# Kernel tuning notes

Measured on AMD Instinct MI355X. Metric: run time of the kernel, lower is better.

## Reference

```python
import jax, jax.numpy as jnp
import numpy as np

NG = 1024      # graphs
NPG = 128      # nodes per graph (forced by lin1 = Linear(128*hid, 128))
N = NG * NPG   # 131072 nodes
DEG = 16       # avg in-graph degree
E = N * DEG    # 2,097,152 edges
IN, H = 4, 64


def setup_inputs() -> dict:
    key = jax.random.key(0)
    ks = jax.random.split(key, 24)
    x = jax.random.normal(ks[0], (N, IN), jnp.float32)
    # edges constrained within each 128-node graph
    src = jax.random.randint(ks[1], (E,), 0, NPG)
    dst = jax.random.randint(ks[2], (E,), 0, NPG)
    off = jnp.repeat(jnp.arange(NG, dtype=jnp.int32) * NPG, NPG * DEG)
    edge_index = jnp.stack([src.astype(jnp.int32) + off, dst.astype(jnp.int32) + off])
    g = lambda k, shp, fan: jax.random.normal(k, shp, jnp.float32) / np.float32(np.sqrt(fan))
    return {
        "x": x, "edge_index": edge_index,
        # GATv2Conv(4->64)
        "Wl": g(ks[3], (IN, H), IN), "bl": jnp.zeros((H,), jnp.float32),
        "Wr": g(ks[4], (IN, H), IN), "br": jnp.zeros((H,), jnp.float32),
        "att_v2": g(ks[5], (H,), H), "b_v2": jnp.zeros((H,), jnp.float32),
        # GATConv #1 (64->64)
        "Wg1": g(ks[6], (H, H), H), "as1": g(ks[7], (H,), H),
        "ad1": g(ks[8], (H,), H), "bg1": jnp.zeros((H,), jnp.float32),
        # GATConv #2 (64->64)
        "Wg2": g(ks[9], (H, H), H), "as2": g(ks[10], (H,), H),
        "ad2": g(ks[11], (H,), H), "bg2": jnp.zeros((H,), jnp.float32),
        # LayerNorm(64)
        "ln_g": jnp.ones((H,), jnp.float32), "ln_b": jnp.zeros((H,), jnp.float32),
        # heads: Linear(128*64 -> 128), Linear(128 -> 1)
        "W1": g(ks[12], (NPG * H, 128), NPG * H), "b1": jnp.zeros((128,), jnp.float32),
        "W2": g(ks[13], (128, 1), 128), "b2": jnp.zeros((1,), jnp.float32),
    }


def _seg_softmax(logits, seg):
    # stable softmax over edges grouped by destination node
    m = jax.ops.segment_max(logits, seg, num_segments=N)
    ex = jnp.exp(logits - m[seg])
    s = jax.ops.segment_sum(ex, seg, num_segments=N)
    return ex / (s[seg] + 1e-16)


def _gatv2(x, src, dst, Wl, bl, Wr, br, att, bias):
    xl = x @ Wl + bl                       # source transform [N,H]
    xr = x @ Wr + br                       # target transform [N,H]
    e = jax.nn.leaky_relu(xl[src] + xr[dst], 0.2) @ att   # [E]
    a = _seg_softmax(e, dst)
    out = jax.ops.segment_sum(a[:, None] * xl[src], dst, num_segments=N)
    return out + bias


def _gat(x, src, dst, W, a_src, a_dst, bias):
    # GATConv default: add self-loops
    loop = jnp.arange(N, dtype=src.dtype)
    s2 = jnp.concatenate([src, loop]); d2 = jnp.concatenate([dst, loop])
    xw = x @ W                             # [N,H]
    al_s = xw @ a_src; al_d = xw @ a_dst   # per-node attention halves [N]
    e = jax.nn.leaky_relu(al_s[s2] + al_d[d2], 0.2)
    a = _seg_softmax(e, d2)
    out = jax.ops.segment_sum(a[:, None] * xw[s2], d2, num_segments=N)
    return out + bias


def _layernorm(x, g, b, eps=1e-5):
    mu = jnp.mean(x, -1, keepdims=True)
    var = jnp.mean(jnp.square(x - mu), -1, keepdims=True)
    return (x - mu) * jax.lax.rsqrt(var + eps) * g + b


def reference(x, edge_index, Wl, bl, Wr, br, att_v2, b_v2,
              Wg1, as1, ad1, bg1, Wg2, as2, ad2, bg2,
              ln_g, ln_b, W1, b1, W2, b2):
    src, dst = edge_index[0], edge_index[1]
    h = jax.nn.leaky_relu(_gatv2(x, src, dst, Wl, bl, Wr, br, att_v2, b_v2), 0.01)
    h = _layernorm(h, ln_g, ln_b)
    h = jax.nn.relu(_gat(h, src, dst, Wg1, as1, ad1, bg1))
    h = jax.nn.relu(_gat(h, src, dst, Wg2, as2, ad2, bg2))
    # linearize: batch is sorted with exactly NPG nodes per graph -> reshape
    h = h.reshape(NG, NPG * H)
    h = jax.nn.leaky_relu(h @ W1 + b1, 0.01)
    return jax.nn.sigmoid(h @ W2 + b2)     # [NG, 1]
```

## Files before the change

### kernel.cpp

```cpp
#include <hip/hip_runtime.h>
#include <hip/hip_bf16.h>

#define NGRAPH 1024
#define NPG 128
#define NTOT (NGRAPH*NPG)
#define EPG 2048
#define ETOT (NTOT*16)
#define HD 64

typedef unsigned int uint;
typedef unsigned short ushort_t;
typedef __attribute__((ext_vector_type(8))) short s8v;
typedef __attribute__((ext_vector_type(4))) float f32x4;

#define MFMA16 __builtin_amdgcn_mfma_f32_16x16x32_bf16

__device__ __forceinline__ float lrelu(float x, float s){ return fmaxf(x, x*s); }
__device__ __forceinline__ float b2lo(uint u){ return __uint_as_float(u << 16); }
__device__ __forceinline__ float b2hi(uint u){ return __uint_as_float(u & 0xFFFF0000u); }
__device__ __forceinline__ uint pkbf(float a, float b){
  union { __hip_bfloat162 h; uint u; } t;
  t.h = __hip_bfloat162{__float2bfloat16(a), __float2bfloat16(b)};
  return t.u;
}
__device__ __forceinline__ ushort_t bfb(float v){
  __hip_bfloat16 h = __float2bfloat16(v);
  union { __hip_bfloat16 h; ushort_t u; } t; t.h = h; return t.u;
}
union U4S8 { uint4 u; s8v s; };
__device__ __forceinline__ s8v bcs8(uint4 u){ U4S8 t; t.u = u; return t.s; }
__device__ __forceinline__ s8v pk8(uint4 x, uint4 y){
  U4S8 t;
  t.u.x = pkbf(__uint_as_float(x.x), __uint_as_float(x.y));
  t.u.y = pkbf(__uint_as_float(x.z), __uint_as_float(x.w));
  t.u.z = pkbf(__uint_as_float(y.x), __uint_as_float(y.y));
  t.u.w = pkbf(__uint_as_float(y.z), __uint_as_float(y.w));
  return t.s;
}

#define DPP_ADD(v, ctrl) ((v) + __int_as_float(__builtin_amdgcn_update_dpp(0, __float_as_int(v), (ctrl), 0xF, 0xF, false)))

__device__ __forceinline__ int oswz(int r, int p){ return (r<<5) | ((((p>>2) ^ (r & 7))<<2) | (p & 3)); }
__device__ __forceinline__ int obase(int r, int oc){ return (r<<5) | (((oc) ^ (r & 7))<<2); }
__device__ __forceinline__ int t64(int r, int p){ return (r<<6) | ((((p>>2) ^ (r & 15))<<2) | (p & 3)); }
__device__ __forceinline__ int t64b(int r, int q){ return (r<<6) | (((q ^ (r & 15))<<2)); }
__device__ __forceinline__ int fP(int r, int k){ return (r<<7) | (((((k>>2) ^ r) & 31)<<2) | (k & 3)); }
__device__ __forceinline__ int fPb(int r, int q){ return (r<<7) | ((((q ^ r) & 31))<<2); }

#define O_A   0
#define O_B   4096
#define O_P   8192
#define O_E   12288
#define O_ED  14336
#define O_SOF 15360
#define O_SPO 15489
#define O_NMV 15617
#define O_SSE 15745
#define O_ALS 15873
#define O_ALD 16001
#define O_WAS 16132
#define O_WAD 16196
#define SM_SZ 16260

__global__ __launch_bounds__(256) void gnn_fused(
    const float* __restrict__ x, const int* __restrict__ ei,
    const float* __restrict__ Wl, const float* __restrict__ bl,
    const float* __restrict__ Wr, const float* __restrict__ br,
    const float* __restrict__ att, const float* __restrict__ bv2,
    const float* __restrict__ Wg1, const float* __restrict__ as1,
    const float* __restrict__ ad1, const float* __restrict__ bg1,
    const float* __restrict__ Wg2, const float* __restrict__ as2,
    const float* __restrict__ ad2, const float* __restrict__ bg2,
    const float* __restrict__ lng, const float* __restrict__ lnb,
    uint* __restrict__ hout)
{
  __shared__ uint SM[SM_SZ];
  uint*     sXl  = SM + O_A;
  uint*     sXr  = SM + O_B;
  float*    Pf   = (float*)(SM + O_P);
  float*    eva  = (float*)(SM + O_E);
  ushort_t* edsd = (ushort_t*)(SM + O_ED);
  int*      soff = (int*)(SM + O_SOF);
  int*      spos = (int*)(SM + O_SPO);
  float*    nmv  = (float*)(SM + O_NMV);
  float*    sse  = (float*)(SM + O_SSE);
  float*    als  = (float*)(SM + O_ALS);
  float*    ald  = (float*)(SM + O_ALD);
  float*    was  = (float*)(SM + O_WAS);
  float*    wad  = (float*)(SM + O_WAD);
  ushort_t* sH16 = (ushort_t*)(SM + O_A);
  ushort_t* sT16 = (ushort_t*)(SM + O_B);
  ushort_t* wg16 = (ushort_t*)(SM + O_E);

  const int g    = blockIdx.x;
  const int tid  = threadIdx.x;
  const int lane = tid & 63;
  const int wv   = tid >> 6;
  const int lw   = lane & 15;
  const int lq   = lane >> 4;
  const int oc   = lane & 7;
  const int ebase = g * EPG;

  if (tid < NPG) spos[tid] = 0;
  __syncthreads();
  for (int e = tid; e < EPG; e += 256)
    atomicAdd(&spos[ei[ETOT + ebase + e] - g*NPG], 1);
  __syncthreads();
  if (wv == 0) {
    int c0 = spos[lane], c1 = spos[lane + 64];
    #pragma unroll
    for (int o = 1; o < 64; o <<= 1) { int t = __shfl_up(c0, o); if (lane >= o) c0 += t; }
    #pragma unroll
    for (int o = 1; o < 64; o <<= 1) { int t = __shfl_up(c1, o); if (lane >= o) c1 += t; }
    int tot0 = __shfl(c0, 63);
    soff[lane + 1]  = c0;
    soff[lane + 65] = c1 + tot0;
    if (lane == 0) soff[0] = 0;
  }
  __syncthreads();
  if (tid < NPG) spos[tid] = soff[tid];
  __syncthreads();
  for (int e = tid; e < EPG; e += 256) {
    int s = ei[ebase + e] - g*NPG;
    int d = ei[ETOT + ebase + e] - g*NPG;
    int p = atomicAdd(&spos[d], 1);
    edsd[p] = (ushort_t)(s | (d << 8));
  }

  {
    const int pl = lane & 31, hb = lane >> 5;
    const float2 wl0 = *(const float2*)&Wl[0*64 + 2*pl];
    const float2 wl1 = *(const float2*)&Wl[1*64 + 2*pl];
    const float2 wl2 = *(const float2*)&Wl[2*64 + 2*pl];
    const float2 wl3 = *(const float2*)&Wl[3*64 + 2*pl];
    const float2 wr0 = *(const float2*)&Wr[0*64 + 2*pl];
    const float2 wr1 = *(const float2*)&Wr[1*64 + 2*pl];
    const float2 wr2 = *(const float2*)&Wr[2*64 + 2*pl];
    const float2 wr3 = *(const float2*)&Wr[3*64 + 2*pl];
    const float2 blp = *(const float2*)&bl[2*pl];
    const float2 brp = *(const float2*)&br[2*pl];
    const float4* x4 = (const float4*)x + (size_t)g * NPG;
    __syncthreads();
    for (int st = 0; st < 16; st++) {
      int i = st*8 + wv*2 + hb;
      float4 xi = x4[i];
      float l0 = blp.x + xi.x*wl0.x + xi.y*wl1.x + xi.z*wl2.x + xi.w*wl3.x;
      float l1 = blp.y + xi.x*wl0.y + xi.y*wl1.y + xi.z*wl2.y + xi.w*wl3.y;
      float r0 = brp.x + xi.x*wr0.x + xi.y*wr1.x + xi.z*wr2.x + xi.w*wr3.x;
      float r1 = brp.y + xi.x*wr0.y + xi.y*wr1.y + xi.z*wr2.y + xi.w*wr3.y;
      sXl[oswz(i, pl)] = pkbf(l0, l1);
      sXr[oswz(i, pl)] = pkbf(r0, r1);
    }
  }
  __syncthreads();

  {
    const int grp = lane >> 3;
    float4 atA = *(const float4*)&att[oc*8];
    float4 atB = *(const float4*)&att[oc*8 + 4];
    int base = wv * 512;
    for (int stp = 0; stp < 64; stp++) {
      int e  = base + stp*8 + grp;
      int sd = edsd[e];
      int s  = sd & 127, d = sd >> 8;
      uint4 ql = *(uint4*)&sXl[obase(s, oc)];
      uint4 qr = *(uint4*)&sXr[obase(d, oc)];
      float acc, v;
      v = b2lo(ql.x)+b2lo(qr.x); acc  = lrelu(v,0.2f)*atA.x;
      v = b2hi(ql.x)+b2hi(qr.x); acc += lrelu(v,0.2f)*atA.y;
      v = b2lo(ql.y)+b2lo(qr.y); acc += lrelu(v,0.2f)*atA.z;
      v = b2hi(ql.y)+b2hi(qr.y); acc += lrelu(v,0.2f)*atA.w;
      v = b2lo(ql.z)+b2lo(qr.z); acc += lrelu(v,0.2f)*atB.x;
      v = b2hi(ql.z)+b2hi(qr.z); acc += lrelu(v,0.2f)*atB.y;
      v = b2lo(ql.w)+b2lo(qr.w); acc += lrelu(v,0.2f)*atB.z;
      v = b2hi(ql.w)+b2hi(qr.w); acc += lrelu(v,0.2f)*atB.w;
      acc = DPP_ADD(acc, 0x111); acc = DPP_ADD(acc, 0x112); acc = DPP_ADD(acc, 0x114);
      if ((lane & 7) == 7) eva[e] = acc;
    }
  }
  __syncthreads();

  {
    const int g16 = tid >> 4, sl = tid & 15;
    for (int it = 0; it < 8; it++) {
      int d = it*16 + g16;
      int p0 = soff[d], p1 = soff[d+1];
      float m = -1e30f;
      for (int p = p0 + sl; p < p1; p += 16) m = fmaxf(m, eva[p]);
      #pragma unroll
      for (int o = 1; o < 16; o <<= 1) m = fmaxf(m, __shfl_xor(m, o));
      float ssum = 0.f;
      for (int p = p0 + sl; p < p1; p += 16) {
        float ex = __expf(eva[p] - m); ssum += ex; eva[p] = ex;
      }
      #pragma unroll
      for (int o = 1; o < 16; o <<= 1) ssum += __shfl_xor(ssum, o);
      if (sl == 0) nmv[d] = 1.f / (ssum + 1e-16f);
    }
    ushort_t* xl16 = (ushort_t*)(SM + O_A);
    int j = tid & 63, spb = tid >> 6;
    for (int i = 0; i < 16; i++) {
      int sp = spb*16 + i;
      float v0 = __uint_as_float((uint)xl16[oswz(2*sp,   j>>1)*2 + (j&1)] << 16);
      float v1 = __uint_as_float((uint)xl16[oswz(2*sp+1, j>>1)*2 + (j&1)] << 16);
      sXr[t64(j, sp)] = pkbf(v0, v1);
    }
  }
  __syncthreads();

  {
    int n0 = 32*(wv>>1), m0 = 16*(wv&1);
    float bja = bv2[n0 + lw], bjb = bv2[n0 + 16 + lw];
    for (int q = 0; q < 4; q++) {
      #pragma unroll
      for (int i = 0; i < 4; i++) { uint4 z = {0,0,0,0}; *(uint4*)&SM[O_P + (tid + i*256)*4] = z; }
      __syncthreads();
      int p0 = soff[q*32], p1 = soff[q*32 + 32];
      for (int p = p0 + tid; p < p1; p += 256) {
        int sd = edsd[p]; int s = sd & 127, d = sd >> 8;
        atomicAdd(&Pf[fP(d - q*32, s)], eva[p] * nmv[d]);
      }
      __syncthreads();
      f32x4 c0 = {0.f,0.f,0.f,0.f}, c1 = {0.f,0.f,0.f,0.f};
      int row = m0 + lw;
      #pragma unroll
      for (int ks = 0; ks < 4; ks++) {
        int kk = ks*32 + lq*8;
        uint4 f0 = *(uint4*)&Pf[fPb(row, kk>>2)];
        uint4 f1 = *(uint4*)&Pf[fPb(row, (kk>>2)+1)];
        s8v a = pk8(f0, f1);
        s8v b0 = bcs8(*(uint4*)&SM[O_B + t64b(n0 + lw,      kk>>3)]);
        s8v b1 = bcs8(*(uint4*)&SM[O_B + t64b(n0 + 16 + lw, kk>>3)]);
        c0 = MFMA16(a, b0, c0, 0, 0, 0);
        c1 = MFMA16(a, b1, c1, 0, 0, 0);
      }
      int rg0 = q*32 + m0 + lq*4;
      #pragma unroll
      for (int rg = 0; rg < 4; rg++) {
        float v0 = lrelu(c0[rg] + bja, 0.01f);
        float v1 = lrelu(c1[rg] + bjb, 0.01f);
        int jc0 = n0 + lw, jc1 = n0 + 16 + lw;
        sH16[oswz(rg0+rg, jc0>>1)*2 + (jc0&1)] = bfb(v0);
        sH16[oswz(rg0+rg, jc1>>1)*2 + (jc1&1)] = bfb(v1);
      }
      __syncthreads();
    }
  }

  {
    int pl = lane & 31, hb = lane >> 5;
    float2 gv = *(const float2*)&lng[2*pl];
    float2 bv = *(const float2*)&lnb[2*pl];
    for (int it = 0; it < 16; it++) {
      int d = it*8 + wv*2 + hb;
      uint w = SM[O_A + oswz(d, pl)];
      float v0 = b2lo(w), v1 = b2hi(w);
      float s1 = v0 + v1, s2 = v0*v0 + v1*v1;
      #pragma unroll
      for (int o = 1; o < 32; o <<= 1) { s1 += __shfl_xor(s1, o); s2 += __shfl_xor(s2, o); }
      float mu  = s1 * 0.015625f;
      float var = s2 * 0.015625f - mu*mu;
      float rs  = rsqrtf(var + 1e-5f);
      v0 = (v0 - mu)*rs*gv.x + bv.x;
      v1 = (v1 - mu)*rs*gv.y + bv.y;
      SM[O_A + oswz(d, pl)] = pkbf(v0, v1);
    }
  }
  __syncthreads();

  for (int layer = 0; layer < 2; layer++) {
    const float* Wg  = layer ? Wg2 : Wg1;
    const float* avs = layer ? as2 : as1;
    const float* avd = layer ? ad2 : ad1;
    const float* bg  = layer ? bg2 : bg1;

    if (tid < 128) {
      const float* av = (tid < 64) ? avs : avd;
      float* dst = (tid < 64) ? was : wad;
      int k = tid & 63;
      float acc = 0.f;
      #pragma unroll
      for (int jj = 0; jj < 16; jj++) {
        float4 w = *(const float4*)&Wg[k*64 + jj*4];
        float4 a = *(const float4*)&av[jj*4];
        acc += w.x*a.x + w.y*a.y + w.z*a.z + w.w*a.w;
      }
      dst[k] = acc;
    } else {
      int t2 = tid - 128;
      #pragma unroll
      for (int i = 0; i < 8; i++) {
        int idx = t2 + i*128;
        int k = idx >> 4, j4 = (idx & 15)*4;
        float4 w = *(const float4*)&Wg[k*64 + j4];
        wg16[oswz(j4+0, k>>1)*2 + (k&1)] = bfb(w.x);
        wg16[oswz(j4+1, k>>1)*2 + (k&1)] = bfb(w.y);
        wg16[oswz(j4+2, k>>1)*2 + (k&1)] = bfb(w.z);
        wg16[oswz(j4+3, k>>1)*2 + (k&1)] = bfb(w.w);
      }
    }
    __syncthreads();

    {
      int row = 16*wv + lw;
      s8v a0 = bcs8(*(uint4*)&SM[O_E + obase(row, lq)]);
      s8v a1 = bcs8(*(uint4*)&SM[O_E + obase(row, 4+lq)]);
      #pragma unroll
      for (int nt = 0; nt < 8; nt++) {
        int d = nt*16 + lw;
        s8v b0 = bcs8(*(uint4*)&SM[O_A + obase(d, lq)]);
        s8v b1 = bcs8(*(uint4*)&SM[O_A + obase(d, 4+lq)]);
        f32x4 c = {0.f,0.f,0.f,0.f};
        c = MFMA16(a0, b0, c, 0, 0, 0);
        c = MFMA16(a1, b1, c, 0, 0, 0);
        int j0 = 16*wv + lq*4;
        #pragma unroll
        for (int rg = 0; rg < 4; rg++)
          sT16[t64(j0+rg, d>>1)*2 + (d&1)] = bfb(c[rg]);
      }
    }
    __syncthreads();

    {
      float4 ws0 = *(float4*)&was[oc*8], ws1 = *(float4*)&was[oc*8 + 4];
      float4 wd0 = *(float4*)&wad[oc*8], wd1 = *(float4*)&wad[oc*8 + 4];
      for (int ps = 0; ps < 4; ps++) {
        int n = ps*32 + (tid >> 3);
        uint4 q = *(uint4*)&SM[O_A + obase(n, oc)];
        float f0=b2lo(q.x), f1=b2hi(q.x), f2=b2lo(q.y), f3=b2hi(q.y);
        float f4=b2lo(q.z), f5=b2hi(q.z), f6=b2lo(q.w), f7=b2hi(q.w);
        float sa = f0*ws0.x+f1*ws0.y+f2*ws0.z+f3*ws0.w+f4*ws1.x+f5*ws1.y+f6*ws1.z+f7*ws1.w;
        float sd = f0*wd0.x+f1*wd0.y+f2*wd0.z+f3*wd0.w+f4*wd1.x+f5*wd1.y+f6*wd1.z+f7*wd1.w;
        sa = DPP_ADD(sa, 0x111); sa = DPP_ADD(sa, 0x112); sa = DPP_ADD(sa, 0x114);
        sd = DPP_ADD(sd, 0x111); sd = DPP_ADD(sd, 0x112); sd = DPP_ADD(sd, 0x114);
        if ((lane & 7) == 7) { als[n] = sa; ald[n] = sd; }
      }
    }
    __syncthreads();

    #pragma unroll
    for (int i = 0; i < 8; i++) {
      int e = tid + i*256;
      int sd = edsd[e];
      eva[e] = lrelu(als[sd & 127] + ald[sd >> 8], 0.2f);
    }
    __syncthreads();

    {
      const int g16 = tid >> 4, sl = tid & 15;
      for (int it = 0; it < 8; it++) {
        int d = it*16 + g16;
        int p0 = soff[d], p1 = soff[d+1];
        float se = lrelu(als[d] + ald[d], 0.2f);
        float m = se;
        for (int p = p0 + sl; p < p1; p += 16) m = fmaxf(m, eva[p]);
        #pragma unroll
        for (int o = 1; o < 16; o <<= 1) m = fmaxf(m, __shfl_xor(m, o));
        float ex0 = __expf(se - m);
        float ssum = 0.f;
        for (int p = p0 + sl; p < p1; p += 16) {
          float ex = __expf(eva[p] - m); ssum += ex; eva[p] = ex;
        }
        #pragma unroll
        for (int o = 1; o < 16; o <<= 1) ssum += __shfl_xor(ssum, o);
        if (sl == 0) { nmv[d] = 1.f / (ssum + ex0 + 1e-16f); sse[d] = ex0; }
      }
    }
    __syncthreads();

    {
      int n0 = 32*(wv>>1), m0 = 16*(wv&1);
      float bja = bg[n0 + lw], bjb = bg[n0 + 16 + lw];
      for (int q = 0; q < 4; q++) {
        #pragma unroll
        for (int i = 0; i < 4; i++) { uint4 z = {0,0,0,0}; *(uint4*)&SM[O_P + (tid + i*256)*4] = z; }
        __syncthreads();
        int p0 = soff[q*32], p1 = soff[q*32 + 32];
        for (int p = p0 + tid; p < p1; p += 256) {
          int sd = edsd[p]; int s = sd & 127, d = sd >> 8;
          atomicAdd(&Pf[fP(d - q*32, s)], eva[p] * nmv[d]);
        }
        if (tid < 32) { int d = q*32 + tid; atomicAdd(&Pf[fP(tid, d)], sse[d] * nmv[d]); }
        __syncthreads();
        f32x4 c0 = {0.f,0.f,0.f,0.f}, c1 = {0.f,0.f,0.f,0.f};
        int row = m0 + lw;
        #pragma unroll
        for (int ks = 0; ks < 4; ks++) {
          int kk = ks*32 + lq*8;
          uint4 f0 = *(uint4*)&Pf[fPb(row, kk>>2)];
          uint4 f1 = *(uint4*)&Pf[fPb(row, (kk>>2)+1)];
          s8v a = pk8(f0, f1);
          s8v b0 = bcs8(*(uint4*)&SM[O_B + t64b(n0 + lw,      kk>>3)]);
          s8v b1 = bcs8(*(uint4*)&SM[O_B + t64b(n0 + 16 + lw, kk>>3)]);
          c0 = MFMA16(a, b0, c0, 0, 0, 0);
          c1 = MFMA16(a, b1, c1, 0, 0, 0);
        }
        int rg0 = q*32 + m0 + lq*4;
        #pragma unroll
        for (int rg = 0; rg < 4; rg++) {
          float v0 = fmaxf(c0[rg] + bja, 0.f);
          float v1 = fmaxf(c1[rg] + bjb, 0.f);
          int jc0 = n0 + lw, jc1 = n0 + 16 + lw;
          sH16[oswz(rg0+rg, jc0>>1)*2 + (jc0&1)] = bfb(v0);
          sH16[oswz(rg0+rg, jc1>>1)*2 + (jc1&1)] = bfb(v1);
        }
        __syncthreads();
      }
    }
  }

  {
    uint* hg = hout + (size_t)g * 4096;
    #pragma unroll
    for (int i = 0; i < 16; i++) {
      int idx = tid + i*256;
      hg[idx] = SM[O_A + oswz(idx >> 5, idx & 31)];
    }
  }
}

__global__ __launch_bounds__(256) void w1_transpose(const float* __restrict__ W1,
                                                    uint* __restrict__ w1t)
{
  __shared__ float sw[64*130];
  const int tid = threadIdx.x;
  const int k0 = blockIdx.x * 64;
  #pragma unroll
  for (int i = 0; i < 8; i++) {
    int idx = tid + i*256;
    int r = idx >> 5, c4 = (idx & 31)*4;
    *(float4*)&sw[r*130 + c4] = *(const float4*)&W1[(size_t)(k0+r)*128 + c4];
  }
  __syncthreads();
  #pragma unroll
  for (int i = 0; i < 16; i++) {
    int idx = tid + i*256;
    int c = idx >> 5, kp = idx & 31;
    w1t[(size_t)c*4096 + (k0>>1) + kp] = pkbf(sw[(2*kp)*130 + c], sw[(2*kp+1)*130 + c]);
  }
}

__global__ __launch_bounds__(256) void head_gemm(
    const uint* __restrict__ hbuf, const uint* __restrict__ w1t,
    float* __restrict__ partial)
{
  __shared__ uint sAh[2048];
  __shared__ uint sBh[4096];
  const int tid = threadIdx.x, lane = tid & 63, wv = tid >> 6;
  const int lw = lane & 15, lq = lane >> 4;
  const int g0 = blockIdx.x * 64;
  const int ks = blockIdx.y;
  f32x4 acc[8];
  #pragma unroll
  for (int i = 0; i < 8; i++) acc[i] = f32x4{0.f,0.f,0.f,0.f};

  for (int ch = 0; ch < 8; ch++) {
    int pb = ks*256 + ch*32;
    #pragma unroll
    for (int i = 0; i < 2; i++) {
      int idx = tid + i*256; int r = idx >> 3, q4 = idx & 7;
      uint4 v = *(const uint4*)&hbuf[(size_t)(g0+r)*4096 + pb + q4*4];
      *(uint4*)&sAh[(r<<5) | ((q4 ^ (r & 7))<<2)] = v;
    }
    #pragma unroll
    for (int i = 0; i < 4; i++) {
      int idx = tid + i*256; int r = idx >> 3, q4 = idx & 7;
      uint4 v = *(const uint4*)&w1t[(size_t)r*4096 + pb + q4*4];
      *(uint4*)&sBh[(r<<5) | ((q4 ^ (r & 7))<<2)] = v;
    }
    __syncthreads();
    int ra = 16*wv + lw;
    s8v a0 = bcs8(*(uint4*)&sAh[obase(ra, lq)]);
    s8v a1 = bcs8(*(uint4*)&sAh[obase(ra, 4+lq)]);
    #pragma unroll
    for (int nt = 0; nt < 8; nt++) {
      int c = nt*16 + lw;
      s8v b0 = bcs8(*(uint4*)&sBh[obase(c, lq)]);
      s8v b1 = bcs8(*(uint4*)&sBh[obase(c, 4+lq)]);
      acc[nt] = MFMA16(a0, b0, acc[nt], 0, 0, 0);
      acc[nt] = MFMA16(a1, b1, acc[nt], 0, 0, 0);
    }
    __syncthreads();
  }
  float* pp = partial + (size_t)ks*131072;
  #pragma unroll
  for (int nt = 0; nt < 8; nt++) {
    int c = nt*16 + lw;
    int r0 = g0 + 16*wv + lq*4;
    #pragma unroll
    for (int rg = 0; rg < 4; rg++)
      pp[(size_t)(r0+rg)*128 + c] = acc[nt][rg];
  }
}

__global__ __launch_bounds__(64) void head_out(
    const float* __restrict__ partial, const float* __restrict__ b1,
    const float* __restrict__ W2, const float* __restrict__ b2,
    float* __restrict__ out)
{
  const int g = blockIdx.x;
  const int l = threadIdx.x;
  float v0 = b1[l], v1 = b1[64 + l];
  #pragma unroll
  for (int s = 0; s < 16; s++) {
    v0 += partial[(size_t)s*131072 + g*128 + l];
    v1 += partial[(size_t)s*131072 + g*128 + 64 + l];
  }
  float sum = lrelu(v0, 0.01f)*W2[l] + lrelu(v1, 0.01f)*W2[64 + l];
  #pragma unroll
  for (int m = 32; m > 0; m >>= 1) sum += __shfl_xor(sum, m);
  if (l == 0) out[g] = 1.f / (1.f + __expf(-(sum + b2[0])));
}

extern "C" void kernel_launch(void* const* d_in, const int* in_sizes, int n_in,
                              void* d_out, int out_size, void* d_ws, size_t ws_size,
                              hipStream_t stream) {
  const float* x   = (const float*)d_in[0];
  const int*   ei  = (const int*)  d_in[1];
  const float* Wl  = (const float*)d_in[2];
  const float* bl_ = (const float*)d_in[3];
  const float* Wr  = (const float*)d_in[4];
  const float* br_ = (const float*)d_in[5];
  const float* att = (const float*)d_in[6];
  const float* bv2 = (const float*)d_in[7];
  const float* Wg1 = (const float*)d_in[8];
  const float* as1 = (const float*)d_in[9];
  const float* ad1 = (const float*)d_in[10];
  const float* bg1 = (const float*)d_in[11];
  const float* Wg2 = (const float*)d_in[12];
  const float* as2 = (const float*)d_in[13];
  const float* ad2 = (const float*)d_in[14];
  const float* bg2 = (const float*)d_in[15];
  const float* lng = (const float*)d_in[16];
  const float* lnb = (const float*)d_in[17];
  const float* W1  = (const float*)d_in[18];
  const float* b1  = (const float*)d_in[19];
  const float* W2  = (const float*)d_in[20];
  const float* b2  = (const float*)d_in[21];
  float* out = (float*)d_out;

  uint*  hbuf    = (uint*)d_ws;
  float* partial = (float*)((char*)d_ws + (size_t)16*1024*1024);
  uint*  w1t     = (uint*)((char*)d_ws + (size_t)24*1024*1024);

  w1_transpose<<<128, 256, 0, stream>>>(W1, w1t);
  gnn_fused<<<NGRAPH, 256, 0, stream>>>(x, ei, Wl, bl_, Wr, br_, att, bv2,
      Wg1, as1, ad1, bg1, Wg2, as2, ad2, bg2, lng, lnb, hbuf);
  head_gemm<<<dim3(16, 16), 256, 0, stream>>>(hbuf, w1t, partial);
  head_out<<<NGRAPH, 64, 0, stream>>>(partial, b1, W2, b2, out);
}
```

Baseline: 289.7 us.

## Shrink LDS footprint by spilling sorted edges to global and halving P tile

```diff
diff --git a/kernel.cpp b/kernel.cpp
--- a/kernel.cpp
+++ b/kernel.cpp
@@ -3,9 +3,8 @@
 
 #define NGRAPH 1024
 #define NPG 128
-#define NTOT (NGRAPH*NPG)
 #define EPG 2048
-#define ETOT (NTOT*16)
+#define ETOT (NGRAPH*NPG*16)
 #define HD 64
 
 typedef unsigned int uint;
@@ -24,8 +23,7 @@
   return t.u;
 }
 __device__ __forceinline__ ushort_t bfb(float v){
-  __hip_bfloat16 h = __float2bfloat16(v);
-  union { __hip_bfloat16 h; ushort_t u; } t; t.h = h; return t.u;
+  union { __hip_bfloat16 h; ushort_t u; } t; t.h = __float2bfloat16(v); return t.u;
 }
 union U4S8 { uint4 u; s8v s; };
 __device__ __forceinline__ s8v bcs8(uint4 u){ U4S8 t; t.u = u; return t.s; }
@@ -37,32 +35,68 @@
   t.u.w = pkbf(__uint_as_float(y.z), __uint_as_float(y.w));
   return t.s;
 }
-
 #define DPP_ADD(v, ctrl) ((v) + __int_as_float(__builtin_amdgcn_update_dpp(0, __float_as_int(v), (ctrl), 0xF, 0xF, false)))
 
 __device__ __forceinline__ int oswz(int r, int p){ return (r<<5) | ((((p>>2) ^ (r & 7))<<2) | (p & 3)); }
 __device__ __forceinline__ int obase(int r, int oc){ return (r<<5) | (((oc) ^ (r & 7))<<2); }
 __device__ __forceinline__ int t64(int r, int p){ return (r<<6) | ((((p>>2) ^ (r & 15))<<2) | (p & 3)); }
 __device__ __forceinline__ int t64b(int r, int q){ return (r<<6) | (((q ^ (r & 15))<<2)); }
-__device__ __forceinline__ int fP(int r, int k){ return (r<<7) | (((((k>>2) ^ r) & 31)<<2) | (k & 3)); }
-__device__ __forceinline__ int fPb(int r, int q){ return (r<<7) | ((((q ^ r) & 31))<<2); }
-
-#define O_A   0
-#define O_B   4096
+__device__ __forceinline__ int fP16(int r, int k){ return (r<<7) | (((((k>>2) ^ r) & 31)<<2) | (k & 3)); }
+__device__ __forceinline__ int fP16b(int r, int q){ return (r<<7) | ((((q ^ r) & 31))<<2); }
+
+#define O_H   0
+#define O_T   4096
 #define O_P   8192
-#define O_E   12288
-#define O_ED  14336
-#define O_SOF 15360
-#define O_SPO 15489
-#define O_NMV 15617
-#define O_SSE 15745
-#define O_ALS 15873
-#define O_ALD 16001
-#define O_WAS 16132
-#define O_WAD 16196
-#define SM_SZ 16260
-
-__global__ __launch_bounds__(256) void gnn_fused(
+#define O_E   10240
+#define O_SOF 12288
+#define O_ALS 12353
+#define O_ALD 12481
+#define SM_SZ 12609
+
+__device__ __forceinline__ void aggregate_rounds(
+    uint* SM, const ushort_t* soff16, const float* eva, const ushort_t* edsG,
+    const float* selfw, const float* biasp, bool dorelu,
+    int tid, int wv, int lw, int lq)
+{
+  float* Pf = (float*)(SM + O_P);
+  ushort_t* sH16 = (ushort_t*)(SM + O_H);
+  float bj = biasp[16*wv + lw];
+  for (int q = 0; q < 8; q++) {
+    uint4 z = {0,0,0,0};
+    *(uint4*)&SM[O_P + tid*8]     = z;
+    *(uint4*)&SM[O_P + tid*8 + 4] = z;
+    __syncthreads();
+    int p0 = soff16[q*16], p1 = soff16[q*16 + 16];
+    for (int p = p0 + tid; p < p1; p += 256) {
+      int sd = edsG[p];
+      atomicAdd(&Pf[fP16((sd >> 8) - q*16, sd & 127)], eva[p]);
+    }
+    if (selfw && tid < 16)
+      atomicAdd(&Pf[fP16(tid, q*16 + tid)], selfw[q*16 + tid]);
+    __syncthreads();
+    f32x4 c = {0.f,0.f,0.f,0.f};
+    #pragma unroll
+    for (int ks = 0; ks < 4; ks++) {
+      int kk = ks*32 + lq*8;
+      uint4 f0 = *(uint4*)&Pf[fP16b(lw, (kk>>2))];
+      uint4 f1 = *(uint4*)&Pf[fP16b(lw, (kk>>2)+1)];
+      s8v a = pk8(f0, f1);
+      s8v b = bcs8(*(uint4*)&SM[O_T + t64b(16*wv + lw, kk>>3)]);
+      c = MFMA16(a, b, c, 0, 0, 0);
+    }
+    int col = 16*wv + lw;
+    #pragma unroll
+    for (int rg = 0; rg < 4; rg++) {
+      float v = c[rg] + bj;
+      v = dorelu ? fmaxf(v, 0.f) : lrelu(v, 0.01f);
+      int r = q*16 + lq*4 + rg;
+      sH16[oswz(r, col>>1)*2 + (col&1)] = bfb(v);
+    }
+    __syncthreads();
+  }
+}
+
+__global__ __launch_bounds__(256, 3) void gnn_fused(
     const float* __restrict__ x, const int* __restrict__ ei,
     const float* __restrict__ Wl, const float* __restrict__ bl,
     const float* __restrict__ Wr, const float* __restrict__ br,
@@ -72,25 +106,15 @@
     const float* __restrict__ Wg2, const float* __restrict__ as2,
     const float* __restrict__ ad2, const float* __restrict__ bg2,
     const float* __restrict__ lng, const float* __restrict__ lnb,
-    uint* __restrict__ hout)
+    uint* __restrict__ hout, uint* __restrict__ edsd_ws)
 {
   __shared__ uint SM[SM_SZ];
-  uint*     sXl  = SM + O_A;
-  uint*     sXr  = SM + O_B;
-  float*    Pf   = (float*)(SM + O_P);
-  float*    eva  = (float*)(SM + O_E);
-  ushort_t* edsd = (ushort_t*)(SM + O_ED);
-  int*      soff = (int*)(SM + O_SOF);
-  int*      spos = (int*)(SM + O_SPO);
-  float*    nmv  = (float*)(SM + O_NMV);
-  float*    sse  = (float*)(SM + O_SSE);
-  float*    als  = (float*)(SM + O_ALS);
-  float*    ald  = (float*)(SM + O_ALD);
-  float*    was  = (float*)(SM + O_WAS);
-  float*    wad  = (float*)(SM + O_WAD);
-  ushort_t* sH16 = (ushort_t*)(SM + O_A);
-  ushort_t* sT16 = (ushort_t*)(SM + O_B);
-  ushort_t* wg16 = (ushort_t*)(SM + O_E);
+  float*    eva   = (float*)(SM + O_E);
+  ushort_t* soff16= (ushort_t*)(SM + O_SOF);
+  float*    als   = (float*)(SM + O_ALS);
+  float*    ald   = (float*)(SM + O_ALD);
+  ushort_t* sH16  = (ushort_t*)(SM + O_H);
+  ushort_t* sT16  = (ushort_t*)(SM + O_T);
 
   const int g    = blockIdx.x;
   const int tid  = threadIdx.x;
@@ -100,34 +124,44 @@
   const int lq   = lane >> 4;
   const int oc   = lane & 7;
   const int ebase = g * EPG;
-
-  if (tid < NPG) spos[tid] = 0;
-  __syncthreads();
-  for (int e = tid; e < EPG; e += 256)
-    atomicAdd(&spos[ei[ETOT + ebase + e] - g*NPG], 1);
-  __syncthreads();
-  if (wv == 0) {
-    int c0 = spos[lane], c1 = spos[lane + 64];
-    #pragma unroll
-    for (int o = 1; o < 64; o <<= 1) { int t = __shfl_up(c0, o); if (lane >= o) c0 += t; }
-    #pragma unroll
-    for (int o = 1; o < 64; o <<= 1) { int t = __shfl_up(c1, o); if (lane >= o) c1 += t; }
-    int tot0 = __shfl(c0, 63);
-    soff[lane + 1]  = c0;
-    soff[lane + 65] = c1 + tot0;
-    if (lane == 0) soff[0] = 0;
-  }
-  __syncthreads();
-  if (tid < NPG) spos[tid] = soff[tid];
-  __syncthreads();
-  for (int e = tid; e < EPG; e += 256) {
-    int s = ei[ebase + e] - g*NPG;
-    int d = ei[ETOT + ebase + e] - g*NPG;
-    int p = atomicAdd(&spos[d], 1);
-    edsd[p] = (ushort_t)(s | (d << 8));
-  }
+  uint* eg = edsd_ws + (size_t)g * 1024;
+  const ushort_t* edsG = (const ushort_t*)eg;
 
   {
+    int* spos = (int*)(SM + O_P + 1024);
+    ushort_t* edsL = (ushort_t*)(SM + O_P);
+    if (tid < NPG) spos[tid] = 0;
+    __syncthreads();
+    for (int e = tid; e < EPG; e += 256)
+      atomicAdd(&spos[ei[ETOT + ebase + e] - g*NPG], 1);
+    __syncthreads();
+    if (wv == 0) {
+      int c0 = spos[lane], c1 = spos[lane + 64];
+      #pragma unroll
+      for (int o = 1; o < 64; o <<= 1) { int t = __shfl_up(c0, o); if (lane >= o) c0 += t; }
+      #pragma unroll
+      for (int o = 1; o < 64; o <<= 1) { int t = __shfl_up(c1, o); if (lane >= o) c1 += t; }
+      int tot0 = __shfl(c0, 63);
+      soff16[lane + 1]  = (ushort_t)c0;
+      soff16[lane + 65] = (ushort_t)(c1 + tot0);
+      if (lane == 0) soff16[0] = 0;
+    }
+    __syncthreads();
+    if (tid < NPG) spos[tid] = soff16[tid];
+    __syncthreads();
+    for (int e = tid; e < EPG; e += 256) {
+      int s = ei[ebase + e] - g*NPG;
+      int d = ei[ETOT + ebase + e] - g*NPG;
+      int p = atomicAdd(&spos[d], 1);
+      edsL[p] = (ushort_t)(s | (d << 8));
+    }
+    __syncthreads();
+  }
+
+  {
+    #pragma unroll
+    for (int i = 0; i < 4; i++) eg[tid + i*256] = SM[O_P + tid + i*256];
+
     const int pl = lane & 31, hb = lane >> 5;
     const float2 wl0 = *(const float2*)&Wl[0*64 + 2*pl];
     const float2 wl1 = *(const float2*)&Wl[1*64 + 2*pl];
@@ -140,7 +174,6 @@
     const float2 blp = *(const float2*)&bl[2*pl];
     const float2 brp = *(const float2*)&br[2*pl];
     const float4* x4 = (const float4*)x + (size_t)g * NPG;
-    __syncthreads();
     for (int st = 0; st < 16; st++) {
       int i = st*8 + wv*2 + hb;
       float4 xi = x4[i];
@@ -148,23 +181,24 @@
       float l1 = blp.y + xi.x*wl0.y + xi.y*wl1.y + xi.z*wl2.y + xi.w*wl3.y;
       float r0 = brp.x + xi.x*wr0.x + xi.y*wr1.x + xi.z*wr2.x + xi.w*wr3.x;
       float r1 = brp.y + xi.x*wr0.y + xi.y*wr1.y + xi.z*wr2.y + xi.w*wr3.y;
-      sXl[oswz(i, pl)] = pkbf(l0, l1);
-      sXr[oswz(i, pl)] = pkbf(r0, r1);
+      SM[O_H + oswz(i, pl)] = pkbf(l0, l1);
+      SM[O_T + oswz(i, pl)] = pkbf(r0, r1);
     }
   }
   __syncthreads();
 
   {
     const int grp = lane >> 3;
+    const ushort_t* edsL = (const ushort_t*)(SM + O_P);
     float4 atA = *(const float4*)&att[oc*8];
     float4 atB = *(const float4*)&att[oc*8 + 4];
     int base = wv * 512;
     for (int stp = 0; stp < 64; stp++) {
       int e  = base + stp*8 + grp;
-      int sd = edsd[e];
+      int sd = edsL[e];
       int s  = sd & 127, d = sd >> 8;
-      uint4 ql = *(uint4*)&sXl[obase(s, oc)];
-      uint4 qr = *(uint4*)&sXr[obase(d, oc)];
+      uint4 ql = *(uint4*)&SM[O_H + obase(s, oc)];
+      uint4 qr = *(uint4*)&SM[O_T + obase(d, oc)];
       float acc, v;
       v = b2lo(ql.x)+b2lo(qr.x); acc  = lrelu(v,0.2f)*atA.x;
       v = b2hi(ql.x)+b2hi(qr.x); acc += lrelu(v,0.2f)*atA.y;
@@ -184,68 +218,30 @@
     const int g16 = tid >> 4, sl = tid & 15;
     for (int it = 0; it < 8; it++) {
       int d = it*16 + g16;
-      int p0 = soff[d], p1 = soff[d+1];
+      int p0 = soff16[d], p1 = soff16[d+1];
       float m = -1e30f;
       for (int p = p0 + sl; p < p1; p += 16) m = fmaxf(m, eva[p]);
       #pragma unroll
       for (int o = 1; o < 16; o <<= 1) m = fmaxf(m, __shfl_xor(m, o));
       float ssum = 0.f;
-      for (int p = p0 + sl; p < p1; p += 16) {
-        float ex = __expf(eva[p] - m); ssum += ex; eva[p] = ex;
-      }
+      for (int p = p0 + sl; p < p1; p += 16) { float ex = __expf(eva[p]-m); ssum += ex; eva[p] = ex; }
       #pragma unroll
       for (int o = 1; o < 16; o <<= 1) ssum += __shfl_xor(ssum, o);
-      if (sl == 0) nmv[d] = 1.f / (ssum + 1e-16f);
-    }
-    ushort_t* xl16 = (ushort_t*)(SM + O_A);
+      float rnm = 1.f / (ssum + 1e-16f);
+      for (int p = p0 + sl; p < p1; p += 16) eva[p] *= rnm;
+    }
+    ushort_t* xl16 = (ushort_t*)(SM + O_H);
     int j = tid & 63, spb = tid >> 6;
     for (int i = 0; i < 16; i++) {
       int sp = spb*16 + i;
       float v0 = __uint_as_float((uint)xl16[oswz(2*sp,   j>>1)*2 + (j&1)] << 16);
       float v1 = __uint_as_float((uint)xl16[oswz(2*sp+1, j>>1)*2 + (j&1)] << 16);
-      sXr[t64(j, sp)] = pkbf(v0, v1);
+      SM[O_T + t64(j, sp)] = pkbf(v0, v1);
     }
   }
   __syncthreads();
 
-  {
-    int n0 = 32*(wv>>1), m0 = 16*(wv&1);
-    float bja = bv2[n0 + lw], bjb = bv2[n0 + 16 + lw];
-    for (int q = 0; q < 4; q++) {
-      #pragma unroll
-      for (int i = 0; i < 4; i++) { uint4 z = {0,0,0,0}; *(uint4*)&SM[O_P + (tid + i*256)*4] = z; }
-      __syncthreads();
-      int p0 = soff[q*32], p1 = soff[q*32 + 32];
-      for (int p = p0 + tid; p < p1; p += 256) {
-        int sd = edsd[p]; int s = sd & 127, d = sd >> 8;
-        atomicAdd(&Pf[fP(d - q*32, s)], eva[p] * nmv[d]);
-      }
-      __syncthreads();
-      f32x4 c0 = {0.f,0.f,0.f,0.f}, c1 = {0.f,0.f,0.f,0.f};
-      int row = m0 + lw;
-      #pragma unroll
-      for (int ks = 0; ks < 4; ks++) {
-        int kk = ks*32 + lq*8;
-        uint4 f0 = *(uint4*)&Pf[fPb(row, kk>>2)];
-        uint4 f1 = *(uint4*)&Pf[fPb(row, (kk>>2)+1)];
-        s8v a = pk8(f0, f1);
-        s8v b0 = bcs8(*(uint4*)&SM[O_B + t64b(n0 + lw,      kk>>3)]);
-        s8v b1 = bcs8(*(uint4*)&SM[O_B + t64b(n0 + 16 + lw, kk>>3)]);
-        c0 = MFMA16(a, b0, c0, 0, 0, 0);
-        c1 = MFMA16(a, b1, c1, 0, 0, 0);
-      }
-      int rg0 = q*32 + m0 + lq*4;
-      #pragma unroll
-      for (int rg = 0; rg < 4; rg++) {
-        float v0 = lrelu(c0[rg] + bja, 0.01f);
-        float v1 = lrelu(c1[rg] + bjb, 0.01f);
-        int jc0 = n0 + lw, jc1 = n0 + 16 + lw;
-        sH16[oswz(rg0+rg, jc0>>1)*2 + (jc0&1)] = bfb(v0);
-        sH16[oswz(rg0+rg, jc1>>1)*2 + (jc1&1)] = bfb(v1);
-      }
-      __syncthreads();
-    }
-  }
+  aggregate_rounds(SM, soff16, eva, edsG, nullptr, bv2, false, tid, wv, lw, lq);
 
   {
     int pl = lane & 31, hb = lane >> 5;
@@ -253,7 +249,7 @@
     float2 bv = *(const float2*)&lnb[2*pl];
     for (int it = 0; it < 16; it++) {
       int d = it*8 + wv*2 + hb;
-      uint w = SM[O_A + oswz(d, pl)];
+      uint w = SM[O_H + oswz(d, pl)];
       float v0 = b2lo(w), v1 = b2hi(w);
       float s1 = v0 + v1, s2 = v0*v0 + v1*v1;
       #pragma unroll
@@ -261,9 +257,7 @@
       float mu  = s1 * 0.015625f;
       float var = s2 * 0.015625f - mu*mu;
       float rs  = rsqrtf(var + 1e-5f);
-      v0 = (v0 - mu)*rs*gv.x + bv.x;
-      v1 = (v1 - mu)*rs*gv.y + bv.y;
-      SM[O_A + oswz(d, pl)] = pkbf(v0, v1);
+      SM[O_H + oswz(d, pl)] = pkbf((v0-mu)*rs*gv.x + bv.x, (v1-mu)*rs*gv.y + bv.y);
     }
   }
   __syncthreads();
@@ -273,6 +267,9 @@
     const float* avs = layer ? as2 : as1;
     const float* avd = layer ? ad2 : ad1;
     const float* bg  = layer ? bg2 : bg1;
+    float* was = (float*)(SM + O_P);
+    float* wad = was + 64;
+    ushort_t* wg16 = (ushort_t*)(SM + O_E);
 
     if (tid < 128) {
       const float* av = (tid < 64) ? avs : avd;
@@ -308,8 +305,8 @@
       #pragma unroll
       for (int nt = 0; nt < 8; nt++) {
         int d = nt*16 + lw;
-        s8v b0 = bcs8(*(uint4*)&SM[O_A + obase(d, lq)]);
-        s8v b1 = bcs8(*(uint4*)&SM[O_A + obase(d, 4+lq)]);
+        s8v b0 = bcs8(*(uint4*)&SM[O_H + obase(d, lq)]);
+        s8v b1 = bcs8(*(uint4*)&SM[O_H + obase(d, 4+lq)]);
         f32x4 c = {0.f,0.f,0.f,0.f};
         c = MFMA16(a0, b0, c, 0, 0, 0);
         c = MFMA16(a1, b1, c, 0, 0, 0);
@@ -326,7 +323,7 @@
       float4 wd0 = *(float4*)&wad[oc*8], wd1 = *(float4*)&wad[oc*8 + 4];
       for (int ps = 0; ps < 4; ps++) {
         int n = ps*32 + (tid >> 3);
-        uint4 q = *(uint4*)&SM[O_A + obase(n, oc)];
+        uint4 q = *(uint4*)&SM[O_H + obase(n, oc)];
         float f0=b2lo(q.x), f1=b2hi(q.x), f2=b2lo(q.y), f3=b2hi(q.y);
         float f4=b2lo(q.z), f5=b2hi(q.z), f6=b2lo(q.w), f7=b2hi(q.w);
         float sa = f0*ws0.x+f1*ws0.y+f2*ws0.z+f3*ws0.w+f4*ws1.x+f5*ws1.y+f6*ws1.z+f7*ws1.w;
@@ -339,10 +336,12 @@
     __syncthreads();
 
     #pragma unroll
-    for (int i = 0; i < 8; i++) {
-      int e = tid + i*256;
-      int sd = edsd[e];
-      eva[e] = lrelu(als[sd & 127] + ald[sd >> 8], 0.2f);
+    for (int i = 0; i < 4; i++) {
+      uint w = eg[tid + i*256];
+      int e = (tid + i*256)*2;
+      int sd0 = w & 0xFFFF, sd1 = w >> 16;
+      eva[e]   = lrelu(als[sd0 & 127] + ald[sd0 >> 8], 0.2f);
+      eva[e+1] = lrelu(als[sd1 & 127] + ald[sd1 >> 8], 0.2f);
     }
     __syncthreads();
 
@@ -350,7 +349,7 @@
       const int g16 = tid >> 4, sl = tid & 15;
       for (int it = 0; it < 8; it++) {
         int d = it*16 + g16;
-        int p0 = soff[d], p1 = soff[d+1];
+        int p0 = soff16[d], p1 = soff16[d+1];
         float se = lrelu(als[d] + ald[d], 0.2f);
         float m = se;
         for (int p = p0 + sl; p < p1; p += 16) m = fmaxf(m, eva[p]);
@@ -358,55 +357,17 @@
         for (int o = 1; o < 16; o <<= 1) m = fmaxf(m, __shfl_xor(m, o));
         float ex0 = __expf(se - m);
         float ssum = 0.f;
-        for (int p = p0 + sl; p < p1; p += 16) {
-          float ex = __expf(eva[p] - m); ssum += ex; eva[p] = ex;
-        }
+        for (int p = p0 + sl; p < p1; p += 16) { float ex = __expf(eva[p]-m); ssum += ex; eva[p] = ex; }
         #pragma unroll
         for (int o = 1; o < 16; o <<= 1) ssum += __shfl_xor(ssum, o);
-        if (sl == 0) { nmv[d] = 1.f / (ssum + ex0 + 1e-16f); sse[d] = ex0; }
+        float rnm = 1.f / (ssum + ex0 + 1e-16f);
+        for (int p = p0 + sl; p < p1; p += 16) eva[p] *= rnm;
+        if (sl == 0) als[d] = ex0 * rnm;
       }
     }
     __syncthreads();
 
-    {
-      int n0 = 32*(wv>>1), m0 = 16*(wv&1);
-      float bja = bg[n0 + lw], bjb = bg[n0 + 16 + lw];
-      for (int q = 0; q < 4; q++) {
-        #pragma unroll
-        for (int i = 0; i < 4; i++) { uint4 z = {0,0,0,0}; *(uint4*)&SM[O_P + (tid + i*256)*4] = z; }
-        __syncthreads();
-        int p0 = soff[q*32], p1 = soff[q*32 + 32];
-        for (int p = p0 + tid; p < p1; p += 256) {
-          int sd = edsd[p]; int s = sd & 127, d = sd >> 8;
-          atomicAdd(&Pf[fP(d - q*32, s)], eva[p] * nmv[d]);
-        }
-        if (tid < 32) { int d = q*32 + tid; atomicAdd(&Pf[fP(tid, d)], sse[d] * nmv[d]); }
-        __syncthreads();
-        f32x4 c0 = {0.f,0.f,0.f,0.f}, c1 = {0.f,0.f,0.f,0.f};
-        int row = m0 + lw;
-        #pragma unroll
-        for (int ks = 0; ks < 4; ks++) {
-          int kk = ks*32 + lq*8;
-          uint4 f0 = *(uint4*)&Pf[fPb(row, kk>>2)];
-          uint4 f1 = *(uint4*)&Pf[fPb(row, (kk>>2)+1)];
-          s8v a = pk8(f0, f1);
-          s8v b0 = bcs8(*(uint4*)&SM[O_B + t64b(n0 + lw,      kk>>3)]);
-          s8v b1 = bcs8(*(uint4*)&SM[O_B + t64b(n0 + 16 + lw, kk>>3)]);
-          c0 = MFMA16(a, b0, c0, 0, 0, 0);
-          c1 = MFMA16(a, b1, c1, 0, 0, 0);
-        }
-        int rg0 = q*32 + m0 + lq*4;
-        #pragma unroll
-        for (int rg = 0; rg < 4; rg++) {
-          float v0 = fmaxf(c0[rg] + bja, 0.f);
-          float v1 = fmaxf(c1[rg] + bjb, 0.f);
-          int jc0 = n0 + lw, jc1 = n0 + 16 + lw;
-          sH16[oswz(rg0+rg, jc0>>1)*2 + (jc0&1)] = bfb(v0);
-          sH16[oswz(rg0+rg, jc1>>1)*2 + (jc1&1)] = bfb(v1);
-        }
-        __syncthreads();
-      }
-    }
+    aggregate_rounds(SM, soff16, eva, edsG, als, bg, true, tid, wv, lw, lq);
   }
 
   {
@@ -414,7 +375,7 @@
     #pragma unroll
     for (int i = 0; i < 16; i++) {
       int idx = tid + i*256;
-      hg[idx] = SM[O_A + oswz(idx >> 5, idx & 31)];
+      hg[idx] = SM[O_H + oswz(idx >> 5, idx & 31)];
     }
   }
 }
@@ -542,10 +503,11 @@
   uint*  hbuf    = (uint*)d_ws;
   float* partial = (float*)((char*)d_ws + (size_t)16*1024*1024);
   uint*  w1t     = (uint*)((char*)d_ws + (size_t)24*1024*1024);
+  uint*  edsd_ws = (uint*)((char*)d_ws + (size_t)26*1024*1024);
 
   w1_transpose<<<128, 256, 0, stream>>>(W1, w1t);
   gnn_fused<<<NGRAPH, 256, 0, stream>>>(x, ei, Wl, bl_, Wr, br_, att, bv2,
-      Wg1, as1, ad1, bg1, Wg2, as2, ad2, bg2, lng, lnb, hbuf);
+      Wg1, as1, ad1, bg1, Wg2, as2, ad2, bg2, lng, lnb, hbuf, edsd_ws);
   head_gemm<<<dim3(16, 16), 256, 0, stream>>>(hbuf, w1t, partial);
   head_out<<<NGRAPH, 64, 0, stream>>>(partial, b1, W2, b2, out);
 }
```

New measurement: 309.4 us. 1.07x slower.
